# Performance work log

Measured on AMD Instinct MI355X. Metric: run time of the kernel, lower is better.

The kernel has to match this reference:

```python
import jax, jax.numpy as jnp
import numpy as np

B, N, Q = 4, 4096, 4096
K = 32                    # max_neighbors (k = min(max_neighbors, N))
NUM_ATOM_TYPES = 100
EMBED_DIM = 32
RBF_DIM = 16
CUTOFF = 5.0
RBF_GAMMA = 1.0 / max(CUTOFF / max(RBF_DIM, 1), 1e-6) ** 2  # 10.24
EPS = 1e-12


def setup_inputs() -> dict:
    key = jax.random.key(0)
    k1, k2, k3, k4, k5 = jax.random.split(key, 5)
    coords = jax.random.normal(k1, (B, N, 3), dtype=jnp.float32) * 10.0
    atom_types = jax.random.randint(k2, (B, N), 0, NUM_ATOM_TYPES)
    radii = jax.random.uniform(k3, (B, N), dtype=jnp.float32) + 0.5
    query_points = jax.random.normal(k4, (B, Q, 3), dtype=jnp.float32) * 10.0
    atom_mask = jnp.ones((B, N), dtype=bool)
    query_mask = jnp.ones((B, Q), dtype=bool)
    embed_table = jax.random.normal(k5, (NUM_ATOM_TYPES, EMBED_DIM), dtype=jnp.float32)
    rbf_centers = jnp.linspace(0.0, CUTOFF, RBF_DIM, dtype=jnp.float32)
    return {"coords": coords, "atom_types": atom_types, "radii": radii,
            "query_points": query_points, "atom_mask": atom_mask,
            "query_mask": query_mask, "embed_table": embed_table,
            "rbf_centers": rbf_centers}


def reference(coords, atom_types, radii, query_points, atom_mask, query_mask,
              embed_table, rbf_centers):
    b = coords.shape[0]
    # stable pairwise distances [B, Q, N]
    diff = query_points[:, :, None, :] - coords[:, None, :, :]
    dists = jnp.sqrt(jnp.sum(diff * diff, axis=-1) + EPS)
    masked_dists = jnp.where(atom_mask[:, None, :], dists, jnp.inf)
    # smallest-k via top_k on negated distances -> [B, Q, K]
    neg_vals, sorted_indices = jax.lax.top_k(-masked_dists, K)
    sorted_dists = -neg_vals

    bidx = jnp.arange(b)[:, None, None]                       # [B,1,1]
    neighbor_atom_mask = atom_mask[bidx, sorted_indices]      # [B,Q,K]
    neighbor_mask = neighbor_atom_mask & (sorted_dists <= CUTOFF) & query_mask[:, :, None]

    neighbor_coords = coords[bidx, sorted_indices]            # [B,Q,K,3]
    neighbor_radii = radii[bidx, sorted_indices][..., None]   # [B,Q,K,1]
    neighbor_types = atom_types[bidx, sorted_indices]         # [B,Q,K]
    neighbor_emb = embed_table[neighbor_types]                # [B,Q,K,E]

    rel_pos = query_points[:, :, None, :] - neighbor_coords   # [B,Q,K,3]
    rel_dist = sorted_dists[..., None]                        # [B,Q,K,1]
    rbf = jnp.exp(-RBF_GAMMA * (rel_dist - rbf_centers[None, None, None, :]) ** 2)

    features = jnp.concatenate([rel_pos, neighbor_radii, neighbor_emb, rbf, rel_dist], axis=-1)
    features = jnp.where(neighbor_mask[..., None], features, 0.0)

    safe_indices = jnp.where(neighbor_atom_mask, sorted_indices, -1)
    safe_dists = jnp.where(neighbor_mask, sorted_dists, 0.0)
    return features, neighbor_mask, safe_indices, safe_dists
```

## Files before the change

### kernel.cpp

```cpp
#include <hip/hip_runtime.h>
#include <stdint.h>

#define B_ 4
#define N_ 4096
#define Q_ 4096
#define K_ 32
#define E_ 32
#define R_ 16
#define F_ 53

static constexpr int WAVES   = 16;
static constexpr int THREADS = WAVES * 64;
static constexpr int QPB     = 32;
static constexpr int CAP     = 104;
static constexpr int TILE    = K_ * F_;
static constexpr int NSLOT   = 4;
static constexpr int POOLB   = (QPB * CAP * 8 > NSLOT * TILE * 4)
                             ? (QPB * CAP * 8) : (NSLOT * TILE * 4);

__device__ __forceinline__ unsigned int s2bits(float qx, float qy, float qz,
                                               float cx, float cy, float cz) {
    const float dx = __fsub_rn(qx, cx);
    const float dy = __fsub_rn(qy, cy);
    const float dz = __fsub_rn(qz, cz);
    return __float_as_uint(
        __fadd_rn(__fadd_rn(__fmul_rn(dx, dx), __fmul_rn(dy, dy)),
                  __fmul_rn(dz, dz)));
}

__device__ __forceinline__ unsigned int sbits_threshold(unsigned int Ts) {
    const float dT = __fsqrt_rn(__fadd_rn(__uint_as_float(Ts), 1e-12f));
    const float u  = __uint_as_float(__float_as_uint(dT) + 1);
    unsigned int ST = __float_as_uint(__fmul_rn(u, u)) + 2;
    return ST < Ts ? Ts : ST;
}

__device__ __forceinline__ void bitonic_sort64_u32(unsigned int& v, int lane) {
    #pragma unroll
    for (int k = 2; k <= 64; k <<= 1) {
        #pragma unroll
        for (int j = k >> 1; j > 0; j >>= 1) {
            unsigned int o = __shfl_xor(v, j);
            const bool asc = ((lane & k) == 0);
            const bool lower = ((lane & j) == 0);
            unsigned int mn = v < o ? v : o;
            unsigned int mx = v < o ? o : v;
            v = (lower == asc) ? mn : mx;
        }
    }
}

__device__ __forceinline__ void bitonic_sort64_u64(unsigned long long& v, int lane) {
    #pragma unroll
    for (int k = 2; k <= 64; k <<= 1) {
        #pragma unroll
        for (int j = k >> 1; j > 0; j >>= 1) {
            unsigned long long o = __shfl_xor(v, j);
            const bool asc = ((lane & k) == 0);
            const bool lower = ((lane & j) == 0);
            unsigned long long mn = v < o ? v : o;
            unsigned long long mx = v < o ? o : v;
            v = (lower == asc) ? mn : mx;
        }
    }
}

__device__ __forceinline__ void merge64_u64(unsigned long long& best,
                                            unsigned long long c, int lane) {
    unsigned long long rev = __shfl(c, 63 - lane);
    unsigned long long v = best < rev ? best : rev;
    #pragma unroll
    for (int j = 32; j > 0; j >>= 1) {
        unsigned long long o = __shfl_xor(v, j);
        const bool lower = ((lane & j) == 0);
        unsigned long long mn = v < o ? v : o;
        unsigned long long mx = v < o ? o : v;
        v = lower ? mn : mx;
    }
    best = v;
}

__global__ __launch_bounds__(THREADS, 8)
void lfb_kernel(const float* __restrict__ coords,
                const int* __restrict__ atom_types,
                const float* __restrict__ radii,
                const float* __restrict__ qpts,
                const int* __restrict__ atom_mask,
                const int* __restrict__ query_mask,
                const float* __restrict__ embed,
                const float* __restrict__ centers,
                float* __restrict__ out)
{
    __shared__ __align__(16) float sx[N_], sy[N_], sz[N_];
    __shared__ __align__(16) unsigned char pool[POOLB];
    __shared__ int wcnt[QPB];

    const int tid  = threadIdx.x;
    const int lane = tid & 63;
    const int wv   = tid >> 6;
    const int bq0  = blockIdx.x * QPB;
    const int b    = bq0 / Q_;

    for (int i = tid; i < N_; i += THREADS) {
        const float* c = coords + (size_t)(b * N_ + i) * 3;
        const bool mv = atom_mask[b * N_ + i] != 0;
        sx[i] = mv ? c[0] : 1e30f;
        sy[i] = mv ? c[1] : 1e30f;
        sz[i] = mv ? c[2] : 1e30f;
    }
    if (tid < QPB) wcnt[tid] = 0;
    __syncthreads();

    const int qA = bq0 + wv;
    const int qB = bq0 + WAVES + wv;
    const float qxA = qpts[(size_t)qA * 3 + 0];
    const float qyA = qpts[(size_t)qA * 3 + 1];
    const float qzA = qpts[(size_t)qA * 3 + 2];
    const float qxB = qpts[(size_t)qB * 3 + 0];
    const float qyB = qpts[(size_t)qB * 3 + 1];
    const float qzB = qpts[(size_t)qB * 3 + 2];

    unsigned int mnA = 0xFFFFFFFFu, mnB = 0xFFFFFFFFu;
    for (int i = 0; i < N_ / 256; ++i) {
        const int a0 = i * 256 + lane * 4;
        const float4 X = *(const float4*)&sx[a0];
        const float4 Y = *(const float4*)&sy[a0];
        const float4 Z = *(const float4*)&sz[a0];
        unsigned int a0b = s2bits(qxA, qyA, qzA, X.x, Y.x, Z.x);
        unsigned int a1b = s2bits(qxA, qyA, qzA, X.y, Y.y, Z.y);
        unsigned int a2b = s2bits(qxA, qyA, qzA, X.z, Y.z, Z.z);
        unsigned int a3b = s2bits(qxA, qyA, qzA, X.w, Y.w, Z.w);
        unsigned int b0b = s2bits(qxB, qyB, qzB, X.x, Y.x, Z.x);
        unsigned int b1b = s2bits(qxB, qyB, qzB, X.y, Y.y, Z.y);
        unsigned int b2b = s2bits(qxB, qyB, qzB, X.z, Y.z, Z.z);
        unsigned int b3b = s2bits(qxB, qyB, qzB, X.w, Y.w, Z.w);
        unsigned int ma = (a0b < a1b ? a0b : a1b);
        unsigned int mb = (a2b < a3b ? a2b : a3b);
        ma = ma < mb ? ma : mb;
        mnA = mnA < ma ? mnA : ma;
        unsigned int na = (b0b < b1b ? b0b : b1b);
        unsigned int nb = (b2b < b3b ? b2b : b3b);
        na = na < nb ? na : nb;
        mnB = mnB < na ? mnB : na;
    }
    bitonic_sort64_u32(mnA, lane);
    bitonic_sort64_u32(mnB, lane);
    const unsigned int STA = sbits_threshold(__shfl(mnA, 31));
    const unsigned int STB = sbits_threshold(__shfl(mnB, 31));

    unsigned long long* cb = reinterpret_cast<unsigned long long*>(pool);
    unsigned long long* cbA = cb + (size_t)wv * CAP;
    unsigned long long* cbB = cb + (size_t)(WAVES + wv) * CAP;
    int* cntAp = &wcnt[wv];
    int* cntBp = &wcnt[WAVES + wv];
    for (int i = 0; i < N_ / 256; ++i) {
        const int a0 = i * 256 + lane * 4;
        const float4 X = *(const float4*)&sx[a0];
        const float4 Y = *(const float4*)&sy[a0];
        const float4 Z = *(const float4*)&sz[a0];
        unsigned int sA[4], sB[4];
        sA[0] = s2bits(qxA, qyA, qzA, X.x, Y.x, Z.x);
        sA[1] = s2bits(qxA, qyA, qzA, X.y, Y.y, Z.y);
        sA[2] = s2bits(qxA, qyA, qzA, X.z, Y.z, Z.z);
        sA[3] = s2bits(qxA, qyA, qzA, X.w, Y.w, Z.w);
        sB[0] = s2bits(qxB, qyB, qzB, X.x, Y.x, Z.x);
        sB[1] = s2bits(qxB, qyB, qzB, X.y, Y.y, Z.y);
        sB[2] = s2bits(qxB, qyB, qzB, X.z, Y.z, Z.z);
        sB[3] = s2bits(qxB, qyB, qzB, X.w, Y.w, Z.w);
        #pragma unroll
        for (int j = 0; j < 4; ++j) {
            if (sA[j] <= STA) {
                const int slot = atomicAdd(cntAp, 1);
                if (slot < CAP)
                    cbA[slot] = ((unsigned long long)sA[j] << 32)
                              | (unsigned int)(a0 + j);
            }
            if (sB[j] <= STB) {
                const int slot = atomicAdd(cntBp, 1);
                if (slot < CAP)
                    cbB[slot] = ((unsigned long long)sB[j] << 32)
                              | (unsigned int)(a0 + j);
            }
        }
    }
    const int cntA = *cntAp;
    const int cntB = *cntBp;

    auto select_top32 = [&](const unsigned long long* cbuf, int cnt,
                            float qx, float qy, float qz) -> unsigned long long {
        if (cnt <= CAP) {
            unsigned long long best = ~0ull;
            const int nch = (cnt + 63) >> 6;
            for (int c = 0; c < nch; ++c) {
                const int slot = c * 64 + lane;
                unsigned long long v = ~0ull;
                if (slot < cnt) {
                    const unsigned long long raw = cbuf[slot];
                    const float s = __uint_as_float((unsigned int)(raw >> 32));
                    const float d = __fsqrt_rn(__fadd_rn(s, 1e-12f));
                    v = ((unsigned long long)__float_as_uint(d) << 32)
                      | (unsigned int)(raw & 0xFFFFFFFFull);
                }
                bitonic_sort64_u64(v, lane);
                if (c == 0) best = v;
                else        merge64_u64(best, v, lane);
            }
            return best;
        }
        unsigned long long key = ~0ull;
        for (int base = 0; base < N_; base += 64) {
            const int a = base + lane;
            const unsigned int sb = s2bits(qx, qy, qz, sx[a], sy[a], sz[a]);
            const float d = __fsqrt_rn(__fadd_rn(__uint_as_float(sb), 1e-12f));
            unsigned long long cand =
                ((unsigned long long)__float_as_uint(d) << 32) | (unsigned int)a;
            const unsigned long long T = __shfl(key, 31);
            unsigned long long m = __ballot(cand < T);
            while (m) {
                const int src = __ffsll(m) - 1;
                m &= m - 1;
                const unsigned long long nk = __shfl(cand, src);
                const unsigned long long up = __shfl_up(key, 1);
                if (lane < K_) {
                    const unsigned long long repl =
                        (lane == 0) ? nk : (up <= nk ? nk : up);
                    key = (key <= nk) ? key : repl;
                }
            }
        }
        return key;
    };

    const unsigned long long keyA = select_top32(cbA, cntA, qxA, qyA, qzA);
    const unsigned long long keyB = select_top32(cbB, cntB, qxB, qyB, qzB);

    const size_t BQK = (size_t)B_ * Q_ * K_;
    float* out_feat = out;
    float* out_mask = out + BQK * (size_t)F_;
    float* out_idx  = out_mask + BQK;
    float* out_dist = out_idx + BQK;

    const bool qmA = query_mask[qA] != 0;
    const bool qmB = query_mask[qB] != 0;

    if (lane < K_) {
        {
            const float d = __uint_as_float((unsigned int)(keyA >> 32));
            const int  id = (int)(keyA & 0xFFFFFFFFull);
            const bool am = ((unsigned int)(keyA >> 32)) < 0x7F800000u;
            const bool nm = am && (d <= 5.0f) && qmA;
            const size_t o = (size_t)qA * K_ + lane;
            out_mask[o] = nm ? 1.0f : 0.0f;
            out_idx[o]  = am ? (float)id : -1.0f;
            out_dist[o] = nm ? d : 0.0f;
        }
        {
            const float d = __uint_as_float((unsigned int)(keyB >> 32));
            const int  id = (int)(keyB & 0xFFFFFFFFull);
            const bool am = ((unsigned int)(keyB >> 32)) < 0x7F800000u;
            const bool nm = am && (d <= 5.0f) && qmB;
            const size_t o = (size_t)qB * K_ + lane;
            out_mask[o] = nm ? 1.0f : 0.0f;
            out_idx[o]  = am ? (float)id : -1.0f;
            out_dist[o] = nm ? d : 0.0f;
        }
    }

    __syncthreads();

    auto build_and_store = [&](int q, unsigned long long key,
                               float qx, float qy, float qz, bool qm,
                               float* slotp) {
        const float d_l  = __uint_as_float((unsigned int)(key >> 32));
        const int   id_l = (int)(key & 0xFFFFFFFFull) & (N_ - 1);
        const bool  am_l = ((unsigned int)(key >> 32)) < 0x7F800000u;
        const bool  nm_l = am_l && (d_l <= 5.0f) && qm;

        if (lane < K_) {
            float* f = slotp + lane * F_;
            f[0] = nm_l ? __fsub_rn(qx, sx[id_l]) : 0.0f;
            f[1] = nm_l ? __fsub_rn(qy, sy[id_l]) : 0.0f;
            f[2] = nm_l ? __fsub_rn(qz, sz[id_l]) : 0.0f;
            f[3] = nm_l ? radii[b * N_ + id_l] : 0.0f;

            const int t = atom_types[b * N_ + id_l];
            const float4* er4 = (const float4*)(embed + t * E_);
            #pragma unroll
            for (int e = 0; e < E_ / 4; ++e) {
                const float4 v = er4[e];
                f[4 + e * 4 + 0] = nm_l ? v.x : 0.0f;
                f[4 + e * 4 + 1] = nm_l ? v.y : 0.0f;
                f[4 + e * 4 + 2] = nm_l ? v.z : 0.0f;
                f[4 + e * 4 + 3] = nm_l ? v.w : 0.0f;
            }

            const float NG = -(float)(256.0 / 25.0);
            #pragma unroll
            for (int rr = 0; rr < R_; ++rr) {
                const float dd = __fsub_rn(d_l, centers[rr]);
                const float a2 = __fmul_rn(dd, dd);
                f[36 + rr] = nm_l ? expf(__fmul_rn(NG, a2)) : 0.0f;
            }
            f[52] = nm_l ? d_l : 0.0f;
        }
        const float4* s4 = (const float4*)slotp;
        float4* d4 = (float4*)(out_feat + (size_t)q * (size_t)TILE);
        for (int t4 = lane; t4 < TILE / 4; t4 += 64) d4[t4] = s4[t4];
    };

    float* stagef = reinterpret_cast<float*>(pool);
    for (int r = 0; r < 8; ++r) {
        if ((wv >> 2) == (r & 3)) {
            float* slotp = stagef + (size_t)(wv & (NSLOT - 1)) * TILE;
            if (r < 4) build_and_store(qA, keyA, qxA, qyA, qzA, qmA, slotp);
            else       build_and_store(qB, keyB, qxB, qyB, qzB, qmB, slotp);
        }
        __syncthreads();
    }
}

extern "C" void kernel_launch(void* const* d_in, const int* in_sizes, int n_in,
                              void* d_out, int out_size, void* d_ws, size_t ws_size,
                              hipStream_t stream) {
    const float* coords     = (const float*)d_in[0];
    const int*   atom_types = (const int*)d_in[1];
    const float* radii      = (const float*)d_in[2];
    const float* qpts       = (const float*)d_in[3];
    const int*   atom_mask  = (const int*)d_in[4];
    const int*   query_mask = (const int*)d_in[5];
    const float* embed      = (const float*)d_in[6];
    const float* centers    = (const float*)d_in[7];

    dim3 grid((B_ * Q_) / QPB);
    dim3 block(THREADS);
    lfb_kernel<<<grid, block, 0, stream>>>(coords, atom_types, radii, qpts,
                                           atom_mask, query_mask, embed, centers,
                                           (float*)d_out);
}
```

Baseline: 66.98 us.

## Pack distance math into v_pk_f32 ops and use ballot-based candidate compaction

Stores negated atom coordinates so that distance differences become packed adds, and evaluates squared distances two at a time with v_pk_add/mul/fma_f32 inline asm. The per-candidate LDS atomics are replaced with wave ballot/popcount prefix compaction. The buffer now holds only indices, and squared distances are recomputed during selection. The threshold is now a fixed ULP margin on squared distance, and the FMA changes rounding, which could alter which neighbours are selected near ties.

```diff
diff --git a/kernel.cpp b/kernel.cpp
--- a/kernel.cpp
+++ b/kernel.cpp
@@ -15,24 +15,27 @@
 static constexpr int CAP     = 104;
 static constexpr int TILE    = K_ * F_;
 static constexpr int NSLOT   = 4;
-static constexpr int POOLB   = (QPB * CAP * 8 > NSLOT * TILE * 4)
-                             ? (QPB * CAP * 8) : (NSLOT * TILE * 4);
-
-__device__ __forceinline__ unsigned int s2bits(float qx, float qy, float qz,
-                                               float cx, float cy, float cz) {
-    const float dx = __fsub_rn(qx, cx);
-    const float dy = __fsub_rn(qy, cy);
-    const float dz = __fsub_rn(qz, cz);
-    return __float_as_uint(
-        __fadd_rn(__fadd_rn(__fmul_rn(dx, dx), __fmul_rn(dy, dy)),
-                  __fmul_rn(dz, dz)));
-}
-
-__device__ __forceinline__ unsigned int sbits_threshold(unsigned int Ts) {
-    const float dT = __fsqrt_rn(__fadd_rn(__uint_as_float(Ts), 1e-12f));
-    const float u  = __uint_as_float(__float_as_uint(dT) + 1);
-    unsigned int ST = __float_as_uint(__fmul_rn(u, u)) + 2;
-    return ST < Ts ? Ts : ST;
+static constexpr int POOLB   = (QPB * CAP * 4 > NSLOT * TILE * 4)
+                             ? (QPB * CAP * 4) : (NSLOT * TILE * 4);
+
+typedef float v2f __attribute__((ext_vector_type(2)));
+
+__device__ __forceinline__ v2f pk_add(v2f a, v2f b) {
+    v2f d; asm("v_pk_add_f32 %0, %1, %2" : "=v"(d) : "v"(a), "v"(b)); return d;
+}
+__device__ __forceinline__ v2f pk_mul(v2f a, v2f b) {
+    v2f d; asm("v_pk_mul_f32 %0, %1, %2" : "=v"(d) : "v"(a), "v"(b)); return d;
+}
+__device__ __forceinline__ v2f pk_fma(v2f a, v2f b, v2f c) {
+    v2f d; asm("v_pk_fma_f32 %0, %1, %2, %3" : "=v"(d) : "v"(a), "v"(b), "v"(c)); return d;
+}
+
+__device__ __forceinline__ v2f pk_s2(v2f qx, v2f qy, v2f qz,
+                                     v2f nx, v2f ny, v2f nz) {
+    const v2f dx = pk_add(qx, nx);
+    const v2f dy = pk_add(qy, ny);
+    const v2f dz = pk_add(qz, nz);
+    return pk_fma(dz, dz, pk_fma(dy, dy, pk_mul(dx, dx)));
 }
 
 __device__ __forceinline__ void bitonic_sort64_u32(unsigned int& v, int lane) {
@@ -91,9 +94,8 @@
                 const float* __restrict__ centers,
                 float* __restrict__ out)
 {
-    __shared__ __align__(16) float sx[N_], sy[N_], sz[N_];
+    __shared__ __align__(16) float nsx[N_], nsy[N_], nsz[N_];
     __shared__ __align__(16) unsigned char pool[POOLB];
-    __shared__ int wcnt[QPB];
 
     const int tid  = threadIdx.x;
     const int lane = tid & 63;
@@ -104,11 +106,10 @@
     for (int i = tid; i < N_; i += THREADS) {
         const float* c = coords + (size_t)(b * N_ + i) * 3;
         const bool mv = atom_mask[b * N_ + i] != 0;
-        sx[i] = mv ? c[0] : 1e30f;
-        sy[i] = mv ? c[1] : 1e30f;
-        sz[i] = mv ? c[2] : 1e30f;
-    }
-    if (tid < QPB) wcnt[tid] = 0;
+        nsx[i] = mv ? -c[0] : -1e30f;
+        nsy[i] = mv ? -c[1] : -1e30f;
+        nsz[i] = mv ? -c[2] : -1e30f;
+    }
     __syncthreads();
 
     const int qA = bq0 + wv;
@@ -119,74 +120,72 @@
     const float qxB = qpts[(size_t)qB * 3 + 0];
     const float qyB = qpts[(size_t)qB * 3 + 1];
     const float qzB = qpts[(size_t)qB * 3 + 2];
-
-    unsigned int mnA = 0xFFFFFFFFu, mnB = 0xFFFFFFFFu;
+    const v2f qxA2 = {qxA, qxA}, qyA2 = {qyA, qyA}, qzA2 = {qzA, qzA};
+    const v2f qxB2 = {qxB, qxB}, qyB2 = {qyB, qyB}, qzB2 = {qzB, qzB};
+
+    const float INF = __uint_as_float(0x7F800000u);
+    float mA0 = INF, mA1 = INF, mB0 = INF, mB1 = INF;
     for (int i = 0; i < N_ / 256; ++i) {
         const int a0 = i * 256 + lane * 4;
-        const float4 X = *(const float4*)&sx[a0];
-        const float4 Y = *(const float4*)&sy[a0];
-        const float4 Z = *(const float4*)&sz[a0];
-        unsigned int a0b = s2bits(qxA, qyA, qzA, X.x, Y.x, Z.x);
-        unsigned int a1b = s2bits(qxA, qyA, qzA, X.y, Y.y, Z.y);
-        unsigned int a2b = s2bits(qxA, qyA, qzA, X.z, Y.z, Z.z);
-        unsigned int a3b = s2bits(qxA, qyA, qzA, X.w, Y.w, Z.w);
-        unsigned int b0b = s2bits(qxB, qyB, qzB, X.x, Y.x, Z.x);
-        unsigned int b1b = s2bits(qxB, qyB, qzB, X.y, Y.y, Z.y);
-        unsigned int b2b = s2bits(qxB, qyB, qzB, X.z, Y.z, Z.z);
-        unsigned int b3b = s2bits(qxB, qyB, qzB, X.w, Y.w, Z.w);
-        unsigned int ma = (a0b < a1b ? a0b : a1b);
-        unsigned int mb = (a2b < a3b ? a2b : a3b);
-        ma = ma < mb ? ma : mb;
-        mnA = mnA < ma ? mnA : ma;
-        unsigned int na = (b0b < b1b ? b0b : b1b);
-        unsigned int nb = (b2b < b3b ? b2b : b3b);
-        na = na < nb ? na : nb;
-        mnB = mnB < na ? mnB : na;
-    }
+        const float4 X = *(const float4*)&nsx[a0];
+        const float4 Y = *(const float4*)&nsy[a0];
+        const float4 Z = *(const float4*)&nsz[a0];
+        const v2f Xl = {X.x, X.y}, Xh = {X.z, X.w};
+        const v2f Yl = {Y.x, Y.y}, Yh = {Y.z, Y.w};
+        const v2f Zl = {Z.x, Z.y}, Zh = {Z.z, Z.w};
+        const v2f sAl = pk_s2(qxA2, qyA2, qzA2, Xl, Yl, Zl);
+        const v2f sAh = pk_s2(qxA2, qyA2, qzA2, Xh, Yh, Zh);
+        const v2f sBl = pk_s2(qxB2, qyB2, qzB2, Xl, Yl, Zl);
+        const v2f sBh = pk_s2(qxB2, qyB2, qzB2, Xh, Yh, Zh);
+        mA0 = fminf(mA0, fminf(sAl.x, sAh.x));
+        mA1 = fminf(mA1, fminf(sAl.y, sAh.y));
+        mB0 = fminf(mB0, fminf(sBl.x, sBh.x));
+        mB1 = fminf(mB1, fminf(sBl.y, sBh.y));
+    }
+    unsigned int mnA = __float_as_uint(fminf(mA0, mA1));
+    unsigned int mnB = __float_as_uint(fminf(mB0, mB1));
     bitonic_sort64_u32(mnA, lane);
     bitonic_sort64_u32(mnB, lane);
-    const unsigned int STA = sbits_threshold(__shfl(mnA, 31));
-    const unsigned int STB = sbits_threshold(__shfl(mnB, 31));
-
-    unsigned long long* cb = reinterpret_cast<unsigned long long*>(pool);
-    unsigned long long* cbA = cb + (size_t)wv * CAP;
-    unsigned long long* cbB = cb + (size_t)(WAVES + wv) * CAP;
-    int* cntAp = &wcnt[wv];
-    int* cntBp = &wcnt[WAVES + wv];
+    const unsigned int STA = __shfl(mnA, 31) + 64u;
+    const unsigned int STB = __shfl(mnB, 31) + 64u;
+
+    unsigned int* cbA = reinterpret_cast<unsigned int*>(pool) + wv * CAP;
+    unsigned int* cbB = reinterpret_cast<unsigned int*>(pool) + (WAVES + wv) * CAP;
+    const unsigned long long lt = (1ull << lane) - 1ull;
+    int cntA = 0, cntB = 0;
+    auto collect = [&](float s, int idx, unsigned int ST, int& cnt,
+                       unsigned int* cb) {
+        const bool p = __float_as_uint(s) <= ST;
+        const unsigned long long m = __ballot(p);
+        if (p) {
+            const int sl = cnt + __popcll(m & lt);
+            if (sl < CAP) cb[sl] = (unsigned int)idx;
+        }
+        cnt += __popcll(m);
+    };
     for (int i = 0; i < N_ / 256; ++i) {
         const int a0 = i * 256 + lane * 4;
-        const float4 X = *(const float4*)&sx[a0];
-        const float4 Y = *(const float4*)&sy[a0];
-        const float4 Z = *(const float4*)&sz[a0];
-        unsigned int sA[4], sB[4];
-        sA[0] = s2bits(qxA, qyA, qzA, X.x, Y.x, Z.x);
-        sA[1] = s2bits(qxA, qyA, qzA, X.y, Y.y, Z.y);
-        sA[2] = s2bits(qxA, qyA, qzA, X.z, Y.z, Z.z);
-        sA[3] = s2bits(qxA, qyA, qzA, X.w, Y.w, Z.w);
-        sB[0] = s2bits(qxB, qyB, qzB, X.x, Y.x, Z.x);
-        sB[1] = s2bits(qxB, qyB, qzB, X.y, Y.y, Z.y);
-        sB[2] = s2bits(qxB, qyB, qzB, X.z, Y.z, Z.z);
-        sB[3] = s2bits(qxB, qyB, qzB, X.w, Y.w, Z.w);
-        #pragma unroll
-        for (int j = 0; j < 4; ++j) {
-            if (sA[j] <= STA) {
-                const int slot = atomicAdd(cntAp, 1);
-                if (slot < CAP)
-                    cbA[slot] = ((unsigned long long)sA[j] << 32)
-                              | (unsigned int)(a0 + j);
-            }
-            if (sB[j] <= STB) {
-                const int slot = atomicAdd(cntBp, 1);
-                if (slot < CAP)
-                    cbB[slot] = ((unsigned long long)sB[j] << 32)
-                              | (unsigned int)(a0 + j);
-            }
-        }
-    }
-    const int cntA = *cntAp;
-    const int cntB = *cntBp;
-
-    auto select_top32 = [&](const unsigned long long* cbuf, int cnt,
+        const float4 X = *(const float4*)&nsx[a0];
+        const float4 Y = *(const float4*)&nsy[a0];
+        const float4 Z = *(const float4*)&nsz[a0];
+        const v2f Xl = {X.x, X.y}, Xh = {X.z, X.w};
+        const v2f Yl = {Y.x, Y.y}, Yh = {Y.z, Y.w};
+        const v2f Zl = {Z.x, Z.y}, Zh = {Z.z, Z.w};
+        const v2f sAl = pk_s2(qxA2, qyA2, qzA2, Xl, Yl, Zl);
+        const v2f sAh = pk_s2(qxA2, qyA2, qzA2, Xh, Yh, Zh);
+        const v2f sBl = pk_s2(qxB2, qyB2, qzB2, Xl, Yl, Zl);
+        const v2f sBh = pk_s2(qxB2, qyB2, qzB2, Xh, Yh, Zh);
+        collect(sAl.x, a0 + 0, STA, cntA, cbA);
+        collect(sAl.y, a0 + 1, STA, cntA, cbA);
+        collect(sAh.x, a0 + 2, STA, cntA, cbA);
+        collect(sAh.y, a0 + 3, STA, cntA, cbA);
+        collect(sBl.x, a0 + 0, STB, cntB, cbB);
+        collect(sBl.y, a0 + 1, STB, cntB, cbB);
+        collect(sBh.x, a0 + 2, STB, cntB, cbB);
+        collect(sBh.y, a0 + 3, STB, cntB, cbB);
+    }
+
+    auto select_top32 = [&](const unsigned int* cbuf, int cnt,
                             float qx, float qy, float qz) -> unsigned long long {
         if (cnt <= CAP) {
             unsigned long long best = ~0ull;
@@ -195,11 +194,16 @@
                 const int slot = c * 64 + lane;
                 unsigned long long v = ~0ull;
                 if (slot < cnt) {
-                    const unsigned long long raw = cbuf[slot];
-                    const float s = __uint_as_float((unsigned int)(raw >> 32));
+                    const int id = (int)cbuf[slot];
+                    const float dx = __fadd_rn(qx, nsx[id]);
+                    const float dy = __fadd_rn(qy, nsy[id]);
+                    const float dz = __fadd_rn(qz, nsz[id]);
+                    const float s = __fadd_rn(
+                        __fadd_rn(__fmul_rn(dx, dx), __fmul_rn(dy, dy)),
+                        __fmul_rn(dz, dz));
                     const float d = __fsqrt_rn(__fadd_rn(s, 1e-12f));
                     v = ((unsigned long long)__float_as_uint(d) << 32)
-                      | (unsigned int)(raw & 0xFFFFFFFFull);
+                      | (unsigned int)id;
                 }
                 bitonic_sort64_u64(v, lane);
                 if (c == 0) best = v;
@@ -210,8 +214,13 @@
         unsigned long long key = ~0ull;
         for (int base = 0; base < N_; base += 64) {
             const int a = base + lane;
-            const unsigned int sb = s2bits(qx, qy, qz, sx[a], sy[a], sz[a]);
-            const float d = __fsqrt_rn(__fadd_rn(__uint_as_float(sb), 1e-12f));
+            const float dx = __fadd_rn(qx, nsx[a]);
+            const float dy = __fadd_rn(qy, nsy[a]);
+            const float dz = __fadd_rn(qz, nsz[a]);
+            const float s = __fadd_rn(
+                __fadd_rn(__fmul_rn(dx, dx), __fmul_rn(dy, dy)),
+                __fmul_rn(dz, dz));
+            const float d = __fsqrt_rn(__fadd_rn(s, 1e-12f));
             unsigned long long cand =
                 ((unsigned long long)__float_as_uint(d) << 32) | (unsigned int)a;
             const unsigned long long T = __shfl(key, 31);
@@ -278,9 +287,9 @@
 
         if (lane < K_) {
             float* f = slotp + lane * F_;
-            f[0] = nm_l ? __fsub_rn(qx, sx[id_l]) : 0.0f;
-            f[1] = nm_l ? __fsub_rn(qy, sy[id_l]) : 0.0f;
-            f[2] = nm_l ? __fsub_rn(qz, sz[id_l]) : 0.0f;
+            f[0] = nm_l ? __fadd_rn(qx, nsx[id_l]) : 0.0f;
+            f[1] = nm_l ? __fadd_rn(qy, nsy[id_l]) : 0.0f;
+            f[2] = nm_l ? __fadd_rn(qz, nsz[id_l]) : 0.0f;
             f[3] = nm_l ? radii[b * N_ + id_l] : 0.0f;
 
             const int t = atom_types[b * N_ + id_l];
```

Result: faster. 64.66 us (-3.5%).
